# Kernel tuning notes

Hardware: AMD Instinct MI355X
Metric: run time of the kernel (lower is better)

The kernel has to match this reference:

```python
import jax, jax.numpy as jnp
import numpy as np

SCALE = 12000.0        # global `scale` in the source
ACT_LIM = 10000.0
ACT_LIMIT = 10000.0    # self.act_limit
LOG_STD_MIN = -20.0
LOG_STD_MAX = 2.0


def _ste_round(x):
    # straight-through-estimator round (Brevitas-style)
    return x + jax.lax.stop_gradient(jnp.round(x) - x)


def _quant_weight(W):
    # Int8WeightPerTensorFloat: symmetric per-tensor int8 fake-quant
    s = jnp.max(jnp.abs(W)) / 127.0
    Wq = jnp.clip(_ste_round(W / s), -127.0, 127.0) * s
    return Wq, s


def _quant_bias(b, s_bias):
    # Int8Bias: bias scale = input_scale * weight_scale
    return jnp.clip(_ste_round(b / s_bias), -128.0, 127.0) * s_bias


def setup_inputs() -> dict:
    key = jax.random.key(0)
    ks = jax.random.split(key, 8)
    B, OBS, H1, H2, ACT = 32768, 512, 1024, 1024, 64
    obs = jax.random.normal(ks[0], (B, OBS), jnp.float32)
    eps = jax.random.normal(ks[1], (B, ACT), jnp.float32)
    W1 = jax.random.normal(ks[2], (H1, OBS), jnp.float32) * (1.0 / np.sqrt(OBS))
    b1 = jax.random.normal(ks[3], (H1,), jnp.float32) * 0.01
    W2 = jax.random.normal(ks[4], (H2, H1), jnp.float32) * (1.0 / np.sqrt(H1))
    b2 = jax.random.normal(ks[5], (H2,), jnp.float32) * 0.01
    W3 = jax.random.normal(ks[6], (2 * ACT, H2), jnp.float32) * (1.0 / np.sqrt(H2))
    b3 = jax.random.normal(ks[7], (2 * ACT,), jnp.float32) * 0.01
    return {"obs": obs, "eps": eps, "W1": W1, "b1": b1, "W2": W2, "b2": b2, "W3": W3, "b3": b3}


def reference(obs, eps, W1, b1, W2, b2, W3, b3):
    s_in = 1.0 / SCALE
    # quantize_input_tensor: value = (obs * (1/scale) - 0) * (1/scale)
    x = obs * (s_in * s_in)
    # fc1 (int8 weight fake-quant, bias quant with scale = in_scale*w_scale)
    W1q, ws1 = _quant_weight(W1)
    h = jax.nn.relu(x @ W1q.T + _quant_bias(b1, s_in * ws1))
    s1 = s_in * ws1  # QuantReLU(act_quant=None) passes scale through
    # fc2
    W2q, ws2 = _quant_weight(W2)
    h = jax.nn.relu(h @ W2q.T + _quant_bias(b2, s1 * ws2))
    s2 = s1 * ws2
    # fc3
    W3q, ws3 = _quant_weight(W3)
    net_out = h @ W3q.T + _quant_bias(b3, s2 * ws3)  # [B, 2*act_dim]
    mu, log_std = jnp.split(net_out, 2, axis=-1)
    log_std = jnp.clip(log_std, LOG_STD_MIN, LOG_STD_MAX)
    std = jnp.exp(log_std)
    pi = mu + std * eps  # rsample
    # Normal log_prob summed over action dim
    logp = jnp.sum(-0.5 * jnp.square((pi - mu) / std) - log_std - 0.5 * jnp.log(2.0 * jnp.pi), axis=-1)
    # tanh-squash correction
    logp = logp - jnp.sum(2.0 * (jnp.log(2.0) - pi - jax.nn.softplus(-2.0 * pi)), axis=-1)
    action = ACT_LIMIT * jnp.tanh(pi) / ACT_LIM
    return action, logp
```

## Files before the change

kernel.cpp:

```cpp
#include <hip/hip_runtime.h>
#include <math.h>

typedef float f32x4 __attribute__((ext_vector_type(4)));
typedef int   v4i   __attribute__((ext_vector_type(4)));
typedef int   v8i   __attribute__((ext_vector_type(8)));

__device__ __forceinline__ void g2l16(const void* g, void* l) {
    __builtin_amdgcn_global_load_lds(
        (__attribute__((address_space(1))) void*)g,
        (__attribute__((address_space(3))) void*)l,
        16, 0, 0);
}

__device__ __forceinline__ int pk8(float a, float b, int old) {
    return __builtin_amdgcn_cvt_pk_fp8_f32(a, b, old, 0);
}
__device__ __forceinline__ int pk8h(float a, float b, int old) {
    return __builtin_amdgcn_cvt_pk_fp8_f32(a, b, old, 1);
}

__global__ void wprep1(const float* __restrict__ W1, const float* __restrict__ W2,
                       const float* __restrict__ W3, float* __restrict__ pmax) {
    int blk = blockIdx.x;
    const float* w; int n, b, nb;
    if (blk < 128)      { w = W1; n = 524288;  b = blk;       nb = 128; }
    else if (blk < 256) { w = W2; n = 1048576; b = blk - 128; nb = 128; }
    else                { w = W3; n = 131072;  b = blk - 256; nb = 32;  }
    float m = 0.f;
    for (int i = b * 256 + threadIdx.x; i < n; i += nb * 256)
        m = fmaxf(m, fabsf(w[i]));
    #pragma unroll
    for (int off = 32; off; off >>= 1)
        m = fmaxf(m, __shfl_down(m, off));
    __shared__ float sm[4];
    int lane = threadIdx.x & 63, wv = threadIdx.x >> 6;
    if (lane == 0) sm[wv] = m;
    __syncthreads();
    if (threadIdx.x == 0)
        pmax[blockIdx.x] = fmaxf(fmaxf(sm[0], sm[1]), fmaxf(sm[2], sm[3]));
}

__global__ void wprep2(const float* __restrict__ pmax,
                       const float* __restrict__ b1, const float* __restrict__ b2,
                       const float* __restrict__ b3,
                       float* __restrict__ scales,
                       float* __restrict__ b1q, float* __restrict__ b2q, float* __restrict__ b3q) {
    __shared__ float sred[3][4];
    __shared__ float ssc[3];
    int tid = threadIdx.x, lane = tid & 63, wv = tid >> 6;
    float m0 = (tid < 128) ? pmax[tid] : 0.f;
    float m1 = (tid < 128) ? pmax[128 + tid] : 0.f;
    float m2 = (tid < 32)  ? pmax[256 + tid] : 0.f;
    #pragma unroll
    for (int off = 32; off; off >>= 1) {
        m0 = fmaxf(m0, __shfl_down(m0, off));
        m1 = fmaxf(m1, __shfl_down(m1, off));
        m2 = fmaxf(m2, __shfl_down(m2, off));
    }
    if (lane == 0) { sred[0][wv] = m0; sred[1][wv] = m1; sred[2][wv] = m2; }
    __syncthreads();
    if (tid < 3) {
        float mm = fmaxf(fmaxf(sred[tid][0], sred[tid][1]), fmaxf(sred[tid][2], sred[tid][3]));
        float s = mm / 127.0f;
        scales[tid] = s; ssc[tid] = s;
    }
    __syncthreads();
    const float s_in = (float)(1.0 / 12000.0);
    float sb1 = s_in * ssc[0];
    float sb2 = sb1 * ssc[1];
    float sb3 = sb2 * ssc[2];
    for (int i = tid; i < 1024; i += 256) {
        b1q[i] = fminf(fmaxf(rintf(b1[i] / sb1), -128.f), 127.f) * sb1;
        b2q[i] = fminf(fmaxf(rintf(b2[i] / sb2), -128.f), 127.f) * sb2;
    }
    if (tid < 128) b3q[tid] = fminf(fmaxf(rintf(b3[tid] / sb3), -128.f), 127.f) * sb3;
}

__global__ void quant_w_all(const float* __restrict__ W1, const float* __restrict__ W2,
                            const float* __restrict__ W3,
                            unsigned char* __restrict__ W1s, unsigned char* __restrict__ W2s,
                            unsigned char* __restrict__ W3s,
                            const float* __restrict__ scales) {
    int b = blockIdx.x;
    const float* w; unsigned char* o; float s; int base;
    if (b < 256)      { w = W1; o = W1s; s = scales[0]; base = b * 2048; }
    else if (b < 768) { w = W2; o = W2s; s = scales[1]; base = (b - 256) * 2048; }
    else              { w = W3; o = W3s; s = scales[2]; base = (b - 768) * 2048; }
    int i = base + threadIdx.x * 8;
    float4 a = *(const float4*)(w + i);
    float4 c = *(const float4*)(w + i + 4);
    #define QW(x) fminf(fmaxf(fminf(fmaxf(rintf((x) / s), -127.f), 127.f) * s * 1024.f, -448.f), 448.f)
    int lo = pk8(QW(a.x), QW(a.y), 0); lo = pk8h(QW(a.z), QW(a.w), lo);
    int hi = pk8(QW(c.x), QW(c.y), 0); hi = pk8h(QW(c.z), QW(c.w), hi);
    #undef QW
    *(int2*)(o + i) = make_int2(lo, hi);
}

__global__ void cvt_fp8(const float* __restrict__ in, unsigned char* __restrict__ out) {
    int i = (blockIdx.x * blockDim.x + threadIdx.x) * 8;
    float4 a = *(const float4*)(in + i);
    float4 c = *(const float4*)(in + i + 4);
    int lo = pk8(a.x, a.y, 0); lo = pk8h(a.z, a.w, lo);
    int hi = pk8(c.x, c.y, 0); hi = pk8h(c.z, c.w, hi);
    *(int2*)(out + i) = make_int2(lo, hi);
}

template <int LGX>
__global__ __launch_bounds__(256, 2)
void gemm8(const unsigned char* __restrict__ A,
           const unsigned char* __restrict__ Wt,
           const float* __restrict__ bias,
           unsigned char* __restrict__ out,
           float descale, float osc, int N, int K) {
    __shared__ char smem[49152];
    char* lA = smem;
    char* lB = smem + 32768;
    const int tid  = threadIdx.x;
    const int wv   = tid >> 6, lane = tid & 63;
    const int wr   = wv >> 1,  wc   = wv & 1;
    const int l15  = lane & 15, l4  = lane >> 4;
    const int lid  = blockIdx.y * gridDim.x + blockIdx.x;
    const int xcd  = lid & 7;
    const int s    = lid >> 3;
    const int mblk = (s >> LGX) * 8 + xcd;
    const int nblk = s & ((1 << LGX) - 1);
    const size_t rowA0 = (size_t)mblk * 256;
    const size_t rowB0 = (size_t)nblk * 128;
    const unsigned char* Ab = A  + rowA0 * K;
    const unsigned char* Bb = Wt + rowB0 * K;
    const int qsw = ((tid & 7) ^ ((tid >> 3) & 7)) * 16;
    const int srow = tid >> 3;

    f32x4 acc[8][4];
    #pragma unroll
    for (int i = 0; i < 8; ++i)
        #pragma unroll
        for (int j = 0; j < 4; ++j)
            acc[i][j] = f32x4{0.f, 0.f, 0.f, 0.f};

    const int p0 = ((l4 * 2) ^ (l15 & 7)) * 16;
    const int p1 = ((l4 * 2 + 1) ^ (l15 & 7)) * 16;

    for (int k0 = 0; k0 < K; k0 += 128) {
        #pragma unroll
        for (int c = 0; c < 8; ++c)
            g2l16(Ab + (size_t)(c * 32 + srow) * K + k0 + qsw, lA + c * 4096 + tid * 16);
        #pragma unroll
        for (int c = 0; c < 4; ++c)
            g2l16(Bb + (size_t)(c * 32 + srow) * K + k0 + qsw, lB + c * 4096 + tid * 16);
        __syncthreads();
        union { v8i v; v4i h[2]; } bfr[4];
        #pragma unroll
        for (int j = 0; j < 4; ++j) {
            const char* br = lB + (wc * 64 + j * 16 + l15) * 128;
            bfr[j].h[0] = *(const v4i*)(br + p0);
            bfr[j].h[1] = *(const v4i*)(br + p1);
        }
        #pragma unroll
        for (int i = 0; i < 8; ++i) {
            const char* ar = lA + (wr * 128 + i * 16 + l15) * 128;
            union { v8i v; v4i h[2]; } af;
            af.h[0] = *(const v4i*)(ar + p0);
            af.h[1] = *(const v4i*)(ar + p1);
            #pragma unroll
            for (int j = 0; j < 4; ++j)
                acc[i][j] = __builtin_amdgcn_mfma_scale_f32_16x16x128_f8f6f4(
                    af.v, bfr[j].v, acc[i][j], 0, 0, 0, 0x7F7F7F7F, 0, 0x7F7F7F7F);
        }
        __syncthreads();
    }

    float* fS = (float*)smem;
    const int rr = tid >> 2;
    const int cb = (tid & 3) * 32;
    float bvj[4];
    #pragma unroll
    for (int j = 0; j < 4; ++j) bvj[j] = bias[rowB0 + wc * 64 + j * 16 + l15];
    #pragma unroll
    for (int p = 0; p < 4; ++p) {
        __syncthreads();
        if (wr == (p >> 1)) {
            const int ib = (p & 1) * 4;
            #pragma unroll
            for (int ii = 0; ii < 4; ++ii) {
                #pragma unroll
                for (int j = 0; j < 4; ++j) {
                    const int col = wc * 64 + j * 16 + l15;
                    #pragma unroll
                    for (int r = 0; r < 4; ++r) {
                        const int lrow = ii * 16 + l4 * 4 + r;
                        float v = fmaxf(acc[ib + ii][j][r] * descale + bvj[j], 0.f);
                        fS[lrow * 128 + ((((col >> 4) ^ (lrow & 7)) << 4) | (col & 15))] = v;
                    }
                }
            }
        }
        __syncthreads();
        const size_t grow = rowA0 + p * 64 + rr;
        #pragma unroll
        for (int h = 0; h < 2; ++h) {
            const int c0 = cb + h * 16;
            const float* src = fS + rr * 128 + (((c0 >> 4) ^ (rr & 7)) << 4);
            v4i d;
            #pragma unroll
            for (int m = 0; m < 4; ++m) {
                float a0 = fminf(src[m * 4 + 0] * osc, 448.f);
                float a1 = fminf(src[m * 4 + 1] * osc, 448.f);
                float a2 = fminf(src[m * 4 + 2] * osc, 448.f);
                float a3 = fminf(src[m * 4 + 3] * osc, 448.f);
                d[m] = pk8h(a2, a3, pk8(a0, a1, 0));
            }
            *(v4i*)(out + grow * (size_t)N + rowB0 + c0) = d;
        }
    }
}

__global__ __launch_bounds__(256)
void gemm3_fused(const unsigned char* __restrict__ A,
                 const unsigned char* __restrict__ Wt,
                 const float* __restrict__ bias,
                 const float* __restrict__ eps,
                 float* __restrict__ act_out, float* __restrict__ logp_out,
                 float descale, int K) {
    __shared__ char smem[32768];
    char* lA = smem;
    char* lB = smem + 8192;
    float* fmu = (float*)smem;
    float* fls = (float*)(smem + 16384);
    const int tid  = threadIdx.x;
    const int wv   = tid >> 6, lane = tid & 63;
    const int wr   = wv >> 1,  wc   = wv & 1;
    const int l15  = lane & 15, l4  = lane >> 4;
    const size_t rowA0 = (size_t)blockIdx.x * 64;
    const unsigned char* Ab = A + rowA0 * K;
    const int qsw = ((tid & 7) ^ ((tid >> 3) & 7)) * 16;
    const int srow = tid >> 3;
    const int p0 = ((l4 * 2) ^ (l15 & 7)) * 16;
    const int p1 = ((l4 * 2 + 1) ^ (l15 & 7)) * 16;

    f32x4 acc[2][4];
    #pragma unroll
    for (int i = 0; i < 2; ++i)
        #pragma unroll
        for (int j = 0; j < 4; ++j)
            acc[i][j] = f32x4{0.f, 0.f, 0.f, 0.f};

    for (int k0 = 0; k0 < K; k0 += 128) {
        #pragma unroll
        for (int c = 0; c < 2; ++c)
            g2l16(Ab + (size_t)(c * 32 + srow) * K + k0 + qsw, lA + c * 4096 + tid * 16);
        #pragma unroll
        for (int c = 0; c < 4; ++c)
            g2l16(Wt + (size_t)(c * 32 + srow) * K + k0 + qsw, lB + c * 4096 + tid * 16);
        __syncthreads();
        union { v8i v; v4i h[2]; } af[2], bfr[4];
        #pragma unroll
        for (int i = 0; i < 2; ++i) {
            const char* ar = lA + (wr * 32 + i * 16 + l15) * 128;
            af[i].h[0] = *(const v4i*)(ar + p0);
            af[i].h[1] = *(const v4i*)(ar + p1);
        }
        #pragma unroll
        for (int j = 0; j < 4; ++j) {
            const char* br = lB + (wc * 64 + j * 16 + l15) * 128;
            bfr[j].h[0] = *(const v4i*)(br + p0);
            bfr[j].h[1] = *(const v4i*)(br + p1);
        }
        #pragma unroll
        for (int i = 0; i < 2; ++i)
            #pragma unroll
            for (int j = 0; j < 4; ++j)
                acc[i][j] = __builtin_amdgcn_mfma_scale_f32_16x16x128_f8f6f4(
                    af[i].v, bfr[j].v, acc[i][j], 0, 0, 0, 0x7F7F7F7F, 0, 0x7F7F7F7F);
        __syncthreads();
    }

    {
        float* dst = wc ? fls : fmu;
        #pragma unroll
        for (int i = 0; i < 2; ++i) {
            #pragma unroll
            for (int j = 0; j < 4; ++j) {
                int c = j * 16 + l15;
                float bv = bias[wc * 64 + c];
                #pragma unroll
                for (int r = 0; r < 4; ++r) {
                    int lr = wr * 32 + i * 16 + l4 * 4 + r;
                    dst[lr * 64 + ((c + lr) & 63)] = acc[i][j][r] * descale + bv;
                }
            }
        }
    }
    __syncthreads();
    {
        int r = tid >> 2;
        size_t grow = rowA0 + r;
        float lp = 0.f;
        #pragma unroll
        for (int t = 0; t < 16; ++t) {
            int j = (tid & 3) * 16 + t;
            int rot = (j + r) & 63;
            float mu = fmu[r * 64 + rot];
            float ls = fls[r * 64 + rot];
            ls = fminf(fmaxf(ls, -20.f), 2.f);
            float sd = expf(ls);
            float e  = eps[grow * 64 + j];
            float pi = fmaf(sd, e, mu);
            act_out[grow * 64 + j] = tanhf(pi);
            lp += -0.5f * e * e - ls - 0.91893853320467274178f;
            float xn = -2.f * pi;
            float sp = fmaxf(xn, 0.f) + log1pf(expf(-fabsf(xn)));
            lp -= 2.f * (0.69314718055994530942f - pi - sp);
        }
        lp += __shfl_xor(lp, 1);
        lp += __shfl_xor(lp, 2);
        if ((tid & 3) == 0) logp_out[grow] = lp;
    }
}

extern "C" void kernel_launch(void* const* d_in, const int* in_sizes, int n_in,
                              void* d_out, int out_size, void* d_ws, size_t ws_size,
                              hipStream_t stream) {
    const float* obs = (const float*)d_in[0];
    const float* eps = (const float*)d_in[1];
    const float* W1  = (const float*)d_in[2];
    const float* b1  = (const float*)d_in[3];
    const float* W2  = (const float*)d_in[4];
    const float* b2  = (const float*)d_in[5];
    const float* W3  = (const float*)d_in[6];
    const float* b3  = (const float*)d_in[7];
    const int B = 32768, OBS = 512, H1 = 1024, H2 = 1024;

    char* ws = (char*)d_ws;
    unsigned char* x8  = (unsigned char*)(ws);
    unsigned char* h1  = (unsigned char*)(ws + 16777216);
    unsigned char* h2  = (unsigned char*)(ws + 50331648);
    unsigned char* W1s = (unsigned char*)(ws + 83886080);
    unsigned char* W2s = (unsigned char*)(ws + 84410368);
    unsigned char* W3s = (unsigned char*)(ws + 85458944);
    float*         b1q = (float*)(ws + 85590016);
    float*         b2q = (float*)(ws + 85594112);
    float*         b3q = (float*)(ws + 85598208);
    float*         scales = (float*)(ws + 85598720);
    float*         pmax   = (float*)(ws + 85599232);

    wprep1<<<288, 256, 0, stream>>>(W1, W2, W3, pmax);
    wprep2<<<1, 256, 0, stream>>>(pmax, b1, b2, b3, scales, b1q, b2q, b3q);
    quant_w_all<<<832, 256, 0, stream>>>(W1, W2, W3, W1s, W2s, W3s, scales);
    cvt_fp8<<<8192, 256, 0, stream>>>(obs, x8);

    const float desc1 = (float)((1.0 / 12000.0) * (1.0 / 12000.0) / 1024.0);
    const float osc1  = 16777216.f;
    const float desc2 = 1.0f / 17179869184.f;
    const float osc2  = 4194304.f;
    const float desc3 = (float)(1.0 / 4294967296.0);

    gemm8<3><<<dim3(8, 128), 256, 0, stream>>>(x8, W1s, b1q, h1, desc1, osc1, H1, OBS);
    gemm8<3><<<dim3(8, 128), 256, 0, stream>>>(h1, W2s, b2q, h2, desc2, osc2, H2, H1);

    float* act_out  = (float*)d_out;
    float* logp_out = act_out + (size_t)B * 64;
    gemm3_fused<<<512, 256, 0, stream>>>(h2, W3s, b3q, eps, act_out, logp_out, desc3, H2);
}
```

Before: 228.1 us.

## Merge prep kernels into two launches and simplify GEMM epilogue staging

Folds the weight abs-max reduction and the obs-to-fp8 conversion into one launch, and merges scale finalisation, bias quantisation and weight quantisation into a second launch. Each quant block now re-reduces the partial maxima itself, so two launches and a serial single-block kernel go away. The gemm8 epilogue swaps the XOR-swizzled shared staging for a padded stride of 132 and writes 8-byte stores instead of 16-byte ones. gemm3_fused also gets an occupancy hint of 3 blocks per SM. The tradeoffs are redundant pmax reads per block and possibly less efficient global stores in the epilogue.

```diff
diff --git a/kernel.cpp b/kernel.cpp
--- a/kernel.cpp
+++ b/kernel.cpp
@@ -19,90 +19,89 @@
     return __builtin_amdgcn_cvt_pk_fp8_f32(a, b, old, 1);
 }
 
-__global__ void wprep1(const float* __restrict__ W1, const float* __restrict__ W2,
-                       const float* __restrict__ W3, float* __restrict__ pmax) {
-    int blk = blockIdx.x;
-    const float* w; int n, b, nb;
-    if (blk < 128)      { w = W1; n = 524288;  b = blk;       nb = 128; }
-    else if (blk < 256) { w = W2; n = 1048576; b = blk - 128; nb = 128; }
-    else                { w = W3; n = 131072;  b = blk - 256; nb = 32;  }
-    float m = 0.f;
-    for (int i = b * 256 + threadIdx.x; i < n; i += nb * 256)
-        m = fmaxf(m, fabsf(w[i]));
+__global__ void prep_cvt(const float* __restrict__ W1, const float* __restrict__ W2,
+                         const float* __restrict__ W3, float* __restrict__ pmax,
+                         const float* __restrict__ obs, unsigned char* __restrict__ x8) {
+    if (blockIdx.x < 288) {
+        int blk = blockIdx.x;
+        const float* w; int n, b, nb;
+        if (blk < 128)      { w = W1; n = 524288;  b = blk;       nb = 128; }
+        else if (blk < 256) { w = W2; n = 1048576; b = blk - 128; nb = 128; }
+        else                { w = W3; n = 131072;  b = blk - 256; nb = 32;  }
+        float m = 0.f;
+        for (int i = b * 256 + threadIdx.x; i < n; i += nb * 256)
+            m = fmaxf(m, fabsf(w[i]));
+        #pragma unroll
+        for (int off = 32; off; off >>= 1)
+            m = fmaxf(m, __shfl_down(m, off));
+        __shared__ float sm[4];
+        int lane = threadIdx.x & 63, wv = threadIdx.x >> 6;
+        if (lane == 0) sm[wv] = m;
+        __syncthreads();
+        if (threadIdx.x == 0)
+            pmax[blockIdx.x] = fmaxf(fmaxf(sm[0], sm[1]), fmaxf(sm[2], sm[3]));
+    } else {
+        int i = ((blockIdx.x - 288) * 256 + threadIdx.x) * 8;
+        float4 a = *(const float4*)(obs + i);
+        float4 c = *(const float4*)(obs + i + 4);
+        int lo = pk8(a.x, a.y, 0); lo = pk8h(a.z, a.w, lo);
+        int hi = pk8(c.x, c.y, 0); hi = pk8h(c.z, c.w, hi);
+        *(int2*)(x8 + i) = make_int2(lo, hi);
+    }
+}
+
+__device__ __forceinline__ float seg_max(const float* __restrict__ pmax, int base, int cnt,
+                                         float* sm) {
+    int tid = threadIdx.x, lane = tid & 63, wv = tid >> 6;
+    float m = (tid < cnt) ? pmax[base + tid] : 0.f;
     #pragma unroll
     for (int off = 32; off; off >>= 1)
         m = fmaxf(m, __shfl_down(m, off));
-    __shared__ float sm[4];
-    int lane = threadIdx.x & 63, wv = threadIdx.x >> 6;
     if (lane == 0) sm[wv] = m;
     __syncthreads();
-    if (threadIdx.x == 0)
-        pmax[blockIdx.x] = fmaxf(fmaxf(sm[0], sm[1]), fmaxf(sm[2], sm[3]));
-}
-
-__global__ void wprep2(const float* __restrict__ pmax,
-                       const float* __restrict__ b1, const float* __restrict__ b2,
-                       const float* __restrict__ b3,
-                       float* __restrict__ scales,
-                       float* __restrict__ b1q, float* __restrict__ b2q, float* __restrict__ b3q) {
-    __shared__ float sred[3][4];
-    __shared__ float ssc[3];
-    int tid = threadIdx.x, lane = tid & 63, wv = tid >> 6;
-    float m0 = (tid < 128) ? pmax[tid] : 0.f;
-    float m1 = (tid < 128) ? pmax[128 + tid] : 0.f;
-    float m2 = (tid < 32)  ? pmax[256 + tid] : 0.f;
-    #pragma unroll
-    for (int off = 32; off; off >>= 1) {
-        m0 = fmaxf(m0, __shfl_down(m0, off));
-        m1 = fmaxf(m1, __shfl_down(m1, off));
-        m2 = fmaxf(m2, __shfl_down(m2, off));
-    }
-    if (lane == 0) { sred[0][wv] = m0; sred[1][wv] = m1; sred[2][wv] = m2; }
+    float r = fmaxf(fmaxf(sm[0], sm[1]), fmaxf(sm[2], sm[3]));
     __syncthreads();
-    if (tid < 3) {
-        float mm = fmaxf(fmaxf(sred[tid][0], sred[tid][1]), fmaxf(sred[tid][2], sred[tid][3]));
-        float s = mm / 127.0f;
-        scales[tid] = s; ssc[tid] = s;
-    }
-    __syncthreads();
-    const float s_in = (float)(1.0 / 12000.0);
-    float sb1 = s_in * ssc[0];
-    float sb2 = sb1 * ssc[1];
-    float sb3 = sb2 * ssc[2];
-    for (int i = tid; i < 1024; i += 256) {
-        b1q[i] = fminf(fmaxf(rintf(b1[i] / sb1), -128.f), 127.f) * sb1;
-        b2q[i] = fminf(fmaxf(rintf(b2[i] / sb2), -128.f), 127.f) * sb2;
-    }
-    if (tid < 128) b3q[tid] = fminf(fmaxf(rintf(b3[tid] / sb3), -128.f), 127.f) * sb3;
-}
-
-__global__ void quant_w_all(const float* __restrict__ W1, const float* __restrict__ W2,
-                            const float* __restrict__ W3,
-                            unsigned char* __restrict__ W1s, unsigned char* __restrict__ W2s,
-                            unsigned char* __restrict__ W3s,
-                            const float* __restrict__ scales) {
-    int b = blockIdx.x;
-    const float* w; unsigned char* o; float s; int base;
-    if (b < 256)      { w = W1; o = W1s; s = scales[0]; base = b * 2048; }
-    else if (b < 768) { w = W2; o = W2s; s = scales[1]; base = (b - 256) * 2048; }
-    else              { w = W3; o = W3s; s = scales[2]; base = (b - 768) * 2048; }
-    int i = base + threadIdx.x * 8;
-    float4 a = *(const float4*)(w + i);
-    float4 c = *(const float4*)(w + i + 4);
-    #define QW(x) fminf(fmaxf(fminf(fmaxf(rintf((x) / s), -127.f), 127.f) * s * 1024.f, -448.f), 448.f)
-    int lo = pk8(QW(a.x), QW(a.y), 0); lo = pk8h(QW(a.z), QW(a.w), lo);
-    int hi = pk8(QW(c.x), QW(c.y), 0); hi = pk8h(QW(c.z), QW(c.w), hi);
-    #undef QW
-    *(int2*)(o + i) = make_int2(lo, hi);
-}
-
-__global__ void cvt_fp8(const float* __restrict__ in, unsigned char* __restrict__ out) {
-    int i = (blockIdx.x * blockDim.x + threadIdx.x) * 8;
-    float4 a = *(const float4*)(in + i);
-    float4 c = *(const float4*)(in + i + 4);
-    int lo = pk8(a.x, a.y, 0); lo = pk8h(a.z, a.w, lo);
-    int hi = pk8(c.x, c.y, 0); hi = pk8h(c.z, c.w, hi);
-    *(int2*)(out + i) = make_int2(lo, hi);
+    return r;
+}
+
+__global__ void quant_all(const float* __restrict__ W1, const float* __restrict__ W2,
+                          const float* __restrict__ W3,
+                          const float* __restrict__ b1, const float* __restrict__ b2,
+                          const float* __restrict__ b3,
+                          unsigned char* __restrict__ W1s, unsigned char* __restrict__ W2s,
+                          unsigned char* __restrict__ W3s,
+                          float* __restrict__ b1q, float* __restrict__ b2q, float* __restrict__ b3q,
+                          const float* __restrict__ pmax) {
+    __shared__ float sm[4];
+    int b = blockIdx.x, tid = threadIdx.x;
+    if (b < 832) {
+        const float* w; unsigned char* o; int base, pb, pc;
+        if (b < 256)      { w = W1; o = W1s; base = b * 2048;         pb = 0;   pc = 128; }
+        else if (b < 768) { w = W2; o = W2s; base = (b - 256) * 2048; pb = 128; pc = 128; }
+        else              { w = W3; o = W3s; base = (b - 768) * 2048; pb = 256; pc = 32;  }
+        float s = seg_max(pmax, pb, pc, sm) / 127.0f;
+        int i = base + tid * 8;
+        float4 a = *(const float4*)(w + i);
+        float4 c = *(const float4*)(w + i + 4);
+        #define QW(x) fminf(fmaxf(fminf(fmaxf(rintf((x) / s), -127.f), 127.f) * s * 1024.f, -448.f), 448.f)
+        int lo = pk8(QW(a.x), QW(a.y), 0); lo = pk8h(QW(a.z), QW(a.w), lo);
+        int hi = pk8(QW(c.x), QW(c.y), 0); hi = pk8h(QW(c.z), QW(c.w), hi);
+        #undef QW
+        *(int2*)(o + i) = make_int2(lo, hi);
+    } else {
+        float ws1 = seg_max(pmax, 0, 128, sm) / 127.0f;
+        float ws2 = seg_max(pmax, 128, 128, sm) / 127.0f;
+        float ws3 = seg_max(pmax, 256, 32, sm) / 127.0f;
+        const float s_in = (float)(1.0 / 12000.0);
+        float sb1 = s_in * ws1;
+        float sb2 = sb1 * ws2;
+        float sb3 = sb2 * ws3;
+        for (int i = tid; i < 1024; i += 256) {
+            b1q[i] = fminf(fmaxf(rintf(b1[i] / sb1), -128.f), 127.f) * sb1;
+            b2q[i] = fminf(fmaxf(rintf(b2[i] / sb2), -128.f), 127.f) * sb2;
+        }
+        if (tid < 128) b3q[tid] = fminf(fmaxf(rintf(b3[tid] / sb3), -128.f), 127.f) * sb3;
+    }
 }
 
 template <int LGX>
@@ -172,7 +171,7 @@
 
     float* fS = (float*)smem;
     const int rr = tid >> 2;
-    const int cb = (tid & 3) * 32;
+    const int c0 = (tid & 3) * 8;
     float bvj[4];
     #pragma unroll
     for (int j = 0; j < 4; ++j) bvj[j] = bias[rowB0 + wc * 64 + j * 16 + l15];
@@ -189,8 +188,7 @@
                     #pragma unroll
                     for (int r = 0; r < 4; ++r) {
                         const int lrow = ii * 16 + l4 * 4 + r;
-                        float v = fmaxf(acc[ib + ii][j][r] * descale + bvj[j], 0.f);
-                        fS[lrow * 128 + ((((col >> 4) ^ (lrow & 7)) << 4) | (col & 15))] = v;
+                        fS[lrow * 132 + col] = fmaxf(acc[ib + ii][j][r] * descale + bvj[j], 0.f);
                     }
                 }
             }
@@ -198,24 +196,24 @@
         __syncthreads();
         const size_t grow = rowA0 + p * 64 + rr;
         #pragma unroll
-        for (int h = 0; h < 2; ++h) {
-            const int c0 = cb + h * 16;
-            const float* src = fS + rr * 128 + (((c0 >> 4) ^ (rr & 7)) << 4);
-            v4i d;
-            #pragma unroll
-            for (int m = 0; m < 4; ++m) {
-                float a0 = fminf(src[m * 4 + 0] * osc, 448.f);
-                float a1 = fminf(src[m * 4 + 1] * osc, 448.f);
-                float a2 = fminf(src[m * 4 + 2] * osc, 448.f);
-                float a3 = fminf(src[m * 4 + 3] * osc, 448.f);
-                d[m] = pk8h(a2, a3, pk8(a0, a1, 0));
-            }
-            *(v4i*)(out + grow * (size_t)N + rowB0 + c0) = d;
-        }
-    }
-}
-
-__global__ __launch_bounds__(256)
+        for (int m = 0; m < 4; ++m) {
+            const float* src = fS + rr * 132 + c0 + m * 32;
+            float a0 = fminf(src[0] * osc, 448.f);
+            float a1 = fminf(src[1] * osc, 448.f);
+            float a2 = fminf(src[2] * osc, 448.f);
+            float a3 = fminf(src[3] * osc, 448.f);
+            float a4 = fminf(src[4] * osc, 448.f);
+            float a5 = fminf(src[5] * osc, 448.f);
+            float a6 = fminf(src[6] * osc, 448.f);
+            float a7 = fminf(src[7] * osc, 448.f);
+            int lo = pk8h(a2, a3, pk8(a0, a1, 0));
+            int hi = pk8h(a6, a7, pk8(a4, a5, 0));
+            *(int2*)(out + grow * (size_t)N + rowB0 + c0 + m * 32) = make_int2(lo, hi);
+        }
+    }
+}
+
+__global__ __launch_bounds__(256, 3)
 void gemm3_fused(const unsigned char* __restrict__ A,
                  const unsigned char* __restrict__ Wt,
                  const float* __restrict__ bias,
@@ -341,13 +339,11 @@
     float*         b1q = (float*)(ws + 85590016);
     float*         b2q = (float*)(ws + 85594112);
     float*         b3q = (float*)(ws + 85598208);
-    float*         scales = (float*)(ws + 85598720);
-    float*         pmax   = (float*)(ws + 85599232);
-
-    wprep1<<<288, 256, 0, stream>>>(W1, W2, W3, pmax);
-    wprep2<<<1, 256, 0, stream>>>(pmax, b1, b2, b3, scales, b1q, b2q, b3q);
-    quant_w_all<<<832, 256, 0, stream>>>(W1, W2, W3, W1s, W2s, W3s, scales);
-    cvt_fp8<<<8192, 256, 0, stream>>>(obs, x8);
+    float*         pmax = (float*)(ws + 85598720);
+
+    prep_cvt<<<8480, 256, 0, stream>>>(W1, W2, W3, pmax, obs, x8);
+    quant_all<<<833, 256, 0, stream>>>(W1, W2, W3, b1, b2, b3,
+                                       W1s, W2s, W3s, b1q, b2q, b3q, pmax);
 
     const float desc1 = (float)((1.0 / 12000.0) * (1.0 / 12000.0) / 1024.0);
     const float osc1  = 16777216.f;
```

After: 222.0 us. 1.03x faster.
